# Performance work log

Measured on AMD Instinct MI355X. Metric: run time of the kernel, lower is better.

The kernel has to match this reference:

```python
import jax, jax.numpy as jnp
import numpy as np


def setup_inputs() -> dict:
    key = jax.random.key(0)
    k1, k2 = jax.random.split(key)
    n, g, dim, cb_size = 32768, 4, 128, 512
    x = jax.random.normal(k1, (n, g, dim), dtype=jnp.float32)
    code_book = jax.random.normal(k2, (g, cb_size, dim), dtype=jnp.float32)
    return {"x": x, "code_book": code_book}


def reference(x, code_book):
    # x: (n, g, dim); code_book: (g, cb_size, dim)
    x2 = jnp.sum(x * x, axis=-1, keepdims=True)          # (n, g, 1)
    cb2 = jnp.sum(code_book * code_book, axis=-1)        # (g, cb_size)
    cross = jnp.einsum('gkd,ngd->ngk', code_book, x)     # (n, g, cb_size)
    dist = x2 + cb2 - 2.0 * cross                        # (n, g, cb_size)
    index = jnp.argmin(dist, axis=-1, keepdims=True)     # (n, g, 1) int
    one_hot = jax.nn.one_hot(index[..., 0], code_book.shape[1], dtype=dist.dtype)  # (n, g, cb_size)
    x_hat = jnp.einsum('ngk,gkd->ngd', one_hot, code_book)  # (n, g, dim)
    return (x_hat, one_hot, index)
```

## Files before the change

### kernel.cpp

```cpp
#include <hip/hip_runtime.h>
#include <hip/hip_bf16.h>

#define N_TOT 32768
#define G 4
#define DIM 128
#define CB 512
#define BM 32

#define XHAT_OFF   0
#define ONEHOT_OFF ((size_t)N_TOT * G * DIM)
#define IDX_OFF    (ONEHOT_OFF + (size_t)N_TOT * G * CB)

#define CB2_BYTES    ((size_t)G * CB * 4)
#define CBH_OFF      CB2_BYTES
#define CBHALF_BYTES ((size_t)G * CB * DIM * 2)
#define CBL_OFF      (CBH_OFF + CBHALF_BYTES)
#define WS_NEED      (CBL_OFF + CBHALF_BYTES)

typedef _Float16 half8    __attribute__((ext_vector_type(8)));
typedef _Float16 half4    __attribute__((ext_vector_type(4)));
typedef float    floatx16 __attribute__((ext_vector_type(16)));
typedef float    floatx4  __attribute__((ext_vector_type(4)));

__device__ __forceinline__ void split8(floatx4 v0, floatx4 v1, half8& hi, half8& lo) {
    float f[8] = {v0.x, v0.y, v0.z, v0.w, v1.x, v1.y, v1.z, v1.w};
#pragma unroll
    for (int e = 0; e < 8; ++e) {
        _Float16 h = (_Float16)f[e];
        hi[e] = h;
        lo[e] = (_Float16)(f[e] - (float)h);
    }
}

__global__ void cvq_cb2_kernel(const float* __restrict__ cb, float* __restrict__ cb2h) {
    int i = blockIdx.x * 256 + threadIdx.x;
    if (i >= G * CB) return;
    const float4* p = (const float4*)&cb[(size_t)i * DIM];
    float s = 0.f;
#pragma unroll
    for (int j = 0; j < DIM / 4; ++j) {
        float4 v = p[j];
        s += v.x * v.x + v.y * v.y + v.z * v.z + v.w * v.w;
    }
    cb2h[i] = 0.5f * s;
}

__global__ void cvq_cbpack_kernel(const float* __restrict__ cb,
                                  _Float16* __restrict__ cbfh, _Float16* __restrict__ cbfl) {
    int t = blockIdx.x * 256 + threadIdx.x;
    int col    = t & 31;
    int h      = (t >> 5) & 1;
    int ks     = (t >> 6) & 7;
    int colblk = (t >> 9) & 15;
    int g      = t >> 13;
    const float* src = &cb[((size_t)(g * CB + colblk * 32 + col)) * DIM + ks * 16 + h * 8];
    half8 hi, lo;
    split8(*(const floatx4*)src, *(const floatx4*)(src + 4), hi, lo);
    *(half8*)&cbfh[(size_t)t * 8] = hi;
    *(half8*)&cbfl[(size_t)t * 8] = lo;
}

__global__ __launch_bounds__(256, 3) void cvq_main_packed_kernel(
        const float* __restrict__ x,
        const _Float16* __restrict__ cbfh, const _Float16* __restrict__ cbfl,
        const float* __restrict__ cb, const float* __restrict__ cb2h,
        float* __restrict__ out) {

    __shared__ float xs[BM * DIM];
    __shared__ float part_v[4][BM];
    __shared__ int   part_i[4][BM];
    __shared__ int   idxs[BM];

    const int n0   = blockIdx.x * BM;
    const int g    = blockIdx.y;
    const int tid  = threadIdx.x;
    const int wid  = tid >> 6;
    const int lane = tid & 63;
    const int col  = lane & 31;
    const int h    = lane >> 5;

#pragma unroll
    for (int p = 0; p < 4; ++p) {
        int t = tid + p * 256;
        int r = t >> 5;
        int c = t & 31;
        floatx4 v = *(const floatx4*)&x[(((size_t)(n0 + r)) * G + g) * DIM + (c << 2)];
        *(floatx4*)&xs[r * DIM + ((c ^ (r & 7)) << 2)] = v;
    }
    __syncthreads();

    const size_t cb_base = ((size_t)g * 16 + wid * 4) * 4096 + (size_t)lane * 8;

    floatx16 acc[4] = {};

#pragma unroll
    for (int ks = 0; ks < 8; ++ks) {
        const int c0 = ks * 4 + h * 2;
        const int base = col * DIM;
        const int s = col & 7;
        floatx4 xa = *(const floatx4*)&xs[base + ((c0 ^ s) << 2)];
        floatx4 xb = *(const floatx4*)&xs[base + (((c0 + 1) ^ s) << 2)];
        half8 ah, al;
        split8(xa, xb, ah, al);
#pragma unroll
        for (int t = 0; t < 4; ++t) {
            const size_t o = cb_base + (size_t)t * 4096 + ks * 512;
            half8 bh = *(const half8*)&cbfh[o];
            half8 bl = *(const half8*)&cbfl[o];
            acc[t] = __builtin_amdgcn_mfma_f32_32x32x16_f16(ah, bh, acc[t], 0, 0, 0);
            acc[t] = __builtin_amdgcn_mfma_f32_32x32x16_f16(ah, bl, acc[t], 0, 0, 0);
            acc[t] = __builtin_amdgcn_mfma_f32_32x32x16_f16(al, bh, acc[t], 0, 0, 0);
        }
    }

    float c2v[4];
#pragma unroll
    for (int t = 0; t < 4; ++t)
        c2v[t] = cb2h[g * CB + wid * 128 + t * 32 + col];

#pragma unroll
    for (int r = 0; r < 16; ++r) {
        const int row = (r & 3) + 8 * (r >> 2) + 4 * h;
        float bv = c2v[0] - acc[0][r];
        int   bi = wid * 128 + col;
#pragma unroll
        for (int t = 1; t < 4; ++t) {
            float sc = c2v[t] - acc[t][r];
            int   kk = wid * 128 + t * 32 + col;
            if (sc < bv) { bv = sc; bi = kk; }
        }
#pragma unroll
        for (int off = 1; off < 32; off <<= 1) {
            float ov = __shfl_xor(bv, off);
            int   oi = __shfl_xor(bi, off);
            if (ov < bv || (ov == bv && oi < bi)) { bv = ov; bi = oi; }
        }
        if (col == 0) { part_v[wid][row] = bv; part_i[wid][row] = bi; }
    }
    __syncthreads();

    if (tid < BM) {
        float bv = part_v[0][tid];
        int   bi = part_i[0][tid];
#pragma unroll
        for (int w = 1; w < 4; ++w) {
            float pv = part_v[w][tid];
            int   pi = part_i[w][tid];
            if (pv < bv || (pv == bv && pi < bi)) { bv = pv; bi = pi; }
        }
        idxs[tid] = bi;
        out[IDX_OFF + (size_t)(n0 + tid) * G + g] = (float)bi;
    }
    __syncthreads();

    float* out_xhat = out + XHAT_OFF;
    float* out_oh   = out + ONEHOT_OFF;

#pragma unroll
    for (int p = 0; p < 4; ++p) {
        int t  = tid + p * 256;
        int r  = t >> 5;
        int d4 = (t & 31) << 2;
        int k  = idxs[r];
        floatx4 v = *(const floatx4*)&cb[((size_t)g * CB + k) * DIM + d4];
        __builtin_nontemporal_store(v, (floatx4*)&out_xhat[(((size_t)(n0 + r)) * G + g) * DIM + d4]);
    }

#pragma unroll
    for (int p = 0; p < 16; ++p) {
        int t  = tid + p * 256;
        int r  = t >> 7;
        int k4 = (t & 127) << 2;
        int k  = idxs[r];
        floatx4 v;
        v.x = (k4 + 0 == k) ? 1.f : 0.f;
        v.y = (k4 + 1 == k) ? 1.f : 0.f;
        v.z = (k4 + 2 == k) ? 1.f : 0.f;
        v.w = (k4 + 3 == k) ? 1.f : 0.f;
        __builtin_nontemporal_store(v, (floatx4*)&out_oh[(((size_t)(n0 + r)) * G + g) * CB + k4]);
    }
}

#define FBM 64
__global__ __launch_bounds__(256, 2) void cvq_main_kernel(
        const float* __restrict__ x,
        const float* __restrict__ cb,
        const float* __restrict__ cb2h,
        float* __restrict__ out) {

    __shared__ float part_v[4][FBM];
    __shared__ int   part_i[4][FBM];
    __shared__ int   idxs[FBM];

    const int n0   = blockIdx.x * FBM;
    const int g    = blockIdx.y;
    const int tid  = threadIdx.x;
    const int wid  = tid >> 6;
    const int lane = tid & 63;
    const int col  = lane & 31;
    const int h    = lane >> 5;
    const int klo  = h * 8;

    const float* xr0 = &x[(((size_t)(n0 + col)) * G + g) * DIM + klo];
    const float* xr1 = &x[(((size_t)(n0 + 32 + col)) * G + g) * DIM + klo];
    const float* cbr[4];
#pragma unroll
    for (int t = 0; t < 4; ++t)
        cbr[t] = &cb[((size_t)g * CB + wid * 128 + t * 32 + col) * DIM + klo];

    floatx16 acc[2][4] = {};

#pragma unroll
    for (int ks = 0; ks < 8; ++ks) {
        const int d = ks * 16;
        half8 ah[2], al[2];
        split8(*(const floatx4*)(xr0 + d), *(const floatx4*)(xr0 + d + 4), ah[0], al[0]);
        split8(*(const floatx4*)(xr1 + d), *(const floatx4*)(xr1 + d + 4), ah[1], al[1]);
#pragma unroll
        for (int t = 0; t < 4; ++t) {
            half8 bh, bl;
            split8(*(const floatx4*)(cbr[t] + d), *(const floatx4*)(cbr[t] + d + 4), bh, bl);
#pragma unroll
            for (int mt = 0; mt < 2; ++mt) {
                acc[mt][t] = __builtin_amdgcn_mfma_f32_32x32x16_f16(ah[mt], bh, acc[mt][t], 0, 0, 0);
                acc[mt][t] = __builtin_amdgcn_mfma_f32_32x32x16_f16(ah[mt], bl, acc[mt][t], 0, 0, 0);
                acc[mt][t] = __builtin_amdgcn_mfma_f32_32x32x16_f16(al[mt], bh, acc[mt][t], 0, 0, 0);
            }
        }
    }

    float c2v[4];
#pragma unroll
    for (int t = 0; t < 4; ++t)
        c2v[t] = cb2h[g * CB + wid * 128 + t * 32 + col];

#pragma unroll
    for (int mt = 0; mt < 2; ++mt) {
#pragma unroll
        for (int r = 0; r < 16; ++r) {
            const int row = mt * 32 + (r & 3) + 8 * (r >> 2) + 4 * h;
            float bv = c2v[0] - acc[mt][0][r];
            int   bi = wid * 128 + col;
#pragma unroll
            for (int t = 1; t < 4; ++t) {
                float sc = c2v[t] - acc[mt][t][r];
                int   kk = wid * 128 + t * 32 + col;
                if (sc < bv) { bv = sc; bi = kk; }
            }
#pragma unroll
            for (int off = 1; off < 32; off <<= 1) {
                float ov = __shfl_xor(bv, off);
                int   oi = __shfl_xor(bi, off);
                if (ov < bv || (ov == bv && oi < bi)) { bv = ov; bi = oi; }
            }
            if (col == 0) { part_v[wid][row] = bv; part_i[wid][row] = bi; }
        }
    }
    __syncthreads();

    if (tid < FBM) {
        float bv = part_v[0][tid];
        int   bi = part_i[0][tid];
#pragma unroll
        for (int w = 1; w < 4; ++w) {
            float pv = part_v[w][tid];
            int   pi = part_i[w][tid];
            if (pv < bv || (pv == bv && pi < bi)) { bv = pv; bi = pi; }
        }
        idxs[tid] = bi;
        out[IDX_OFF + (size_t)(n0 + tid) * G + g] = (float)bi;
    }
    __syncthreads();

    float* out_xhat = out + XHAT_OFF;
    float* out_oh   = out + ONEHOT_OFF;

#pragma unroll
    for (int p = 0; p < 8; ++p) {
        int t  = tid + p * 256;
        int r  = t >> 5;
        int d4 = (t & 31) << 2;
        int k  = idxs[r];
        floatx4 v = *(const floatx4*)&cb[((size_t)g * CB + k) * DIM + d4];
        __builtin_nontemporal_store(v, (floatx4*)&out_xhat[(((size_t)(n0 + r)) * G + g) * DIM + d4]);
    }

#pragma unroll
    for (int p = 0; p < 32; ++p) {
        int t  = tid + p * 256;
        int r  = t >> 7;
        int k4 = (t & 127) << 2;
        int k  = idxs[r];
        floatx4 v;
        v.x = (k4 + 0 == k) ? 1.f : 0.f;
        v.y = (k4 + 1 == k) ? 1.f : 0.f;
        v.z = (k4 + 2 == k) ? 1.f : 0.f;
        v.w = (k4 + 3 == k) ? 1.f : 0.f;
        __builtin_nontemporal_store(v, (floatx4*)&out_oh[(((size_t)(n0 + r)) * G + g) * CB + k4]);
    }
}

extern "C" void kernel_launch(void* const* d_in, const int* in_sizes, int n_in,
                              void* d_out, int out_size, void* d_ws, size_t ws_size,
                              hipStream_t stream) {
    const float* x  = (const float*)d_in[0];
    const float* cb = (const float*)d_in[1];
    float* out = (float*)d_out;
    char*  ws  = (char*)d_ws;
    float* cb2h = (float*)ws;

    if (ws_size >= WS_NEED) {
        _Float16* cbfh = (_Float16*)(ws + CBH_OFF);
        _Float16* cbfl = (_Float16*)(ws + CBL_OFF);
        cvq_cb2_kernel<<<dim3((G * CB + 255) / 256), dim3(256), 0, stream>>>(cb, cb2h);
        cvq_cbpack_kernel<<<dim3(G * CB * 16 / 256), dim3(256), 0, stream>>>(cb, cbfh, cbfl);
        cvq_main_packed_kernel<<<dim3(N_TOT / BM, G), dim3(256), 0, stream>>>(x, cbfh, cbfl, cb, cb2h, out);
    } else {
        cvq_cb2_kernel<<<dim3((G * CB + 255) / 256), dim3(256), 0, stream>>>(cb, cb2h);
        cvq_main_kernel<<<dim3(N_TOT / FBM, G), dim3(256), 0, stream>>>(x, cb, cb2h, out);
    }
}
```

Before: 154.6 us.

## Convert VQ main kernel to persistent blocks with register-resident codebook and x prefetch

Replaces the one-tile-per-block kernel with a persistent kernel of 64×4 blocks of 512 threads, each looping over 16 row tiles. Codebook fp16 hi/lo fragments are loaded once into registers and reused across all tiles. The next x tile is prefetched into a double-buffered LDS slot during compute. This removes repeated codebook reloads and block launch overhead, at the cost of high register pressure and fewer resident waves to hide store latency.

After: 210.4 us. +36.1%, slower.

```diff
diff --git a/kernel.cpp b/kernel.cpp
--- a/kernel.cpp
+++ b/kernel.cpp
@@ -6,6 +6,8 @@
 #define DIM 128
 #define CB 512
 #define BM 32
+#define NBX 64
+#define IT (N_TOT / BM / NBX)
 
 #define XHAT_OFF   0
 #define ONEHOT_OFF ((size_t)N_TOT * G * DIM)
@@ -18,7 +20,6 @@
 #define WS_NEED      (CBL_OFF + CBHALF_BYTES)
 
 typedef _Float16 half8    __attribute__((ext_vector_type(8)));
-typedef _Float16 half4    __attribute__((ext_vector_type(4)));
 typedef float    floatx16 __attribute__((ext_vector_type(16)));
 typedef float    floatx4  __attribute__((ext_vector_type(4)));
 
@@ -60,124 +61,146 @@
     *(half8*)&cbfl[(size_t)t * 8] = lo;
 }
 
-__global__ __launch_bounds__(256, 3) void cvq_main_packed_kernel(
+__global__ __launch_bounds__(512, 2) void cvq_persist_kernel(
         const float* __restrict__ x,
         const _Float16* __restrict__ cbfh, const _Float16* __restrict__ cbfl,
         const float* __restrict__ cb, const float* __restrict__ cb2h,
         float* __restrict__ out) {
 
-    __shared__ float xs[BM * DIM];
-    __shared__ float part_v[4][BM];
-    __shared__ int   part_i[4][BM];
+    __shared__ float xs[2][BM * DIM];
+    __shared__ float part_v[8][BM];
+    __shared__ int   part_i[8][BM];
     __shared__ int   idxs[BM];
 
-    const int n0   = blockIdx.x * BM;
     const int g    = blockIdx.y;
+    const int bx   = blockIdx.x;
     const int tid  = threadIdx.x;
     const int wid  = tid >> 6;
     const int lane = tid & 63;
     const int col  = lane & 31;
     const int h    = lane >> 5;
 
-#pragma unroll
-    for (int p = 0; p < 4; ++p) {
-        int t = tid + p * 256;
-        int r = t >> 5;
-        int c = t & 31;
-        floatx4 v = *(const floatx4*)&x[(((size_t)(n0 + r)) * G + g) * DIM + (c << 2)];
-        *(floatx4*)&xs[r * DIM + ((c ^ (r & 7)) << 2)] = v;
-    }
-    __syncthreads();
-
-    const size_t cb_base = ((size_t)g * 16 + wid * 4) * 4096 + (size_t)lane * 8;
-
-    floatx16 acc[4] = {};
-
-#pragma unroll
-    for (int ks = 0; ks < 8; ++ks) {
-        const int c0 = ks * 4 + h * 2;
-        const int base = col * DIM;
-        const int s = col & 7;
-        floatx4 xa = *(const floatx4*)&xs[base + ((c0 ^ s) << 2)];
-        floatx4 xb = *(const floatx4*)&xs[base + (((c0 + 1) ^ s) << 2)];
-        half8 ah, al;
-        split8(xa, xb, ah, al);
-#pragma unroll
-        for (int t = 0; t < 4; ++t) {
-            const size_t o = cb_base + (size_t)t * 4096 + ks * 512;
-            half8 bh = *(const half8*)&cbfh[o];
-            half8 bl = *(const half8*)&cbfl[o];
-            acc[t] = __builtin_amdgcn_mfma_f32_32x32x16_f16(ah, bh, acc[t], 0, 0, 0);
-            acc[t] = __builtin_amdgcn_mfma_f32_32x32x16_f16(ah, bl, acc[t], 0, 0, 0);
-            acc[t] = __builtin_amdgcn_mfma_f32_32x32x16_f16(al, bh, acc[t], 0, 0, 0);
-        }
-    }
-
-    float c2v[4];
-#pragma unroll
-    for (int t = 0; t < 4; ++t)
-        c2v[t] = cb2h[g * CB + wid * 128 + t * 32 + col];
-
-#pragma unroll
-    for (int r = 0; r < 16; ++r) {
-        const int row = (r & 3) + 8 * (r >> 2) + 4 * h;
-        float bv = c2v[0] - acc[0][r];
-        int   bi = wid * 128 + col;
-#pragma unroll
-        for (int t = 1; t < 4; ++t) {
-            float sc = c2v[t] - acc[t][r];
-            int   kk = wid * 128 + t * 32 + col;
-            if (sc < bv) { bv = sc; bi = kk; }
-        }
-#pragma unroll
-        for (int off = 1; off < 32; off <<= 1) {
-            float ov = __shfl_xor(bv, off);
-            int   oi = __shfl_xor(bi, off);
-            if (ov < bv || (ov == bv && oi < bi)) { bv = ov; bi = oi; }
-        }
-        if (col == 0) { part_v[wid][row] = bv; part_i[wid][row] = bi; }
-    }
-    __syncthreads();
-
-    if (tid < BM) {
-        float bv = part_v[0][tid];
-        int   bi = part_i[0][tid];
-#pragma unroll
-        for (int w = 1; w < 4; ++w) {
-            float pv = part_v[w][tid];
-            int   pi = part_i[w][tid];
-            if (pv < bv || (pv == bv && pi < bi)) { bv = pv; bi = pi; }
-        }
-        idxs[tid] = bi;
-        out[IDX_OFF + (size_t)(n0 + tid) * G + g] = (float)bi;
-    }
-    __syncthreads();
+    half8 bhf[2][8], blf[2][8];
+#pragma unroll
+    for (int t = 0; t < 2; ++t)
+#pragma unroll
+        for (int ks = 0; ks < 8; ++ks) {
+            const size_t o = ((size_t)(g * 16 + wid * 2 + t)) * 4096 + ks * 512 + (size_t)lane * 8;
+            bhf[t][ks] = *(const half8*)&cbfh[o];
+            blf[t][ks] = *(const half8*)&cbfl[o];
+        }
+
+    const float c2v0 = cb2h[g * CB + wid * 64 + col];
+    const float c2v1 = cb2h[g * CB + wid * 64 + 32 + col];
+
+    const int sr  = tid >> 5;
+    const int sc  = tid & 31;
+    const int ssl = sr * DIM + ((sc ^ (sr & 7)) << 2);
 
     float* out_xhat = out + XHAT_OFF;
     float* out_oh   = out + ONEHOT_OFF;
 
-#pragma unroll
-    for (int p = 0; p < 4; ++p) {
-        int t  = tid + p * 256;
-        int r  = t >> 5;
-        int d4 = (t & 31) << 2;
-        int k  = idxs[r];
-        floatx4 v = *(const floatx4*)&cb[((size_t)g * CB + k) * DIM + d4];
-        __builtin_nontemporal_store(v, (floatx4*)&out_xhat[(((size_t)(n0 + r)) * G + g) * DIM + d4]);
-    }
-
-#pragma unroll
-    for (int p = 0; p < 16; ++p) {
-        int t  = tid + p * 256;
-        int r  = t >> 7;
-        int k4 = (t & 127) << 2;
-        int k  = idxs[r];
-        floatx4 v;
-        v.x = (k4 + 0 == k) ? 1.f : 0.f;
-        v.y = (k4 + 1 == k) ? 1.f : 0.f;
-        v.z = (k4 + 2 == k) ? 1.f : 0.f;
-        v.w = (k4 + 3 == k) ? 1.f : 0.f;
-        __builtin_nontemporal_store(v, (floatx4*)&out_oh[(((size_t)(n0 + r)) * G + g) * CB + k4]);
+    {
+        const float* p = &x[(((size_t)bx * BM + sr) * G + g) * DIM + (sc << 2)];
+        floatx4 s0 = *(const floatx4*)p;
+        floatx4 s1 = *(const floatx4*)(p + (size_t)16 * G * DIM);
+        *(floatx4*)&xs[0][ssl] = s0;
+        *(floatx4*)&xs[0][ssl + 16 * DIM] = s1;
+    }
+    __syncthreads();
+
+    int cur = 0;
+    for (int it = 0; it < IT; ++it) {
+        const size_t n0 = ((size_t)it * NBX + bx) * BM;
+
+        floatx4 s0, s1;
+        if (it + 1 < IT) {
+            const size_t nn = ((size_t)(it + 1) * NBX + bx) * BM;
+            const float* p = &x[((nn + sr) * G + g) * DIM + (sc << 2)];
+            s0 = *(const floatx4*)p;
+            s1 = *(const floatx4*)(p + (size_t)16 * G * DIM);
+        }
+
+        floatx16 acc[2] = {};
+#pragma unroll
+        for (int ks = 0; ks < 8; ++ks) {
+            const int c0 = ks * 4 + h * 2;
+            const int s  = col & 7;
+            const float* xb = &xs[cur][col * DIM];
+            floatx4 xa = *(const floatx4*)&xb[((c0 ^ s) << 2)];
+            floatx4 xc = *(const floatx4*)&xb[(((c0 + 1) ^ s) << 2)];
+            half8 ah, al;
+            split8(xa, xc, ah, al);
+#pragma unroll
+            for (int t = 0; t < 2; ++t) {
+                acc[t] = __builtin_amdgcn_mfma_f32_32x32x16_f16(ah, bhf[t][ks], acc[t], 0, 0, 0);
+                acc[t] = __builtin_amdgcn_mfma_f32_32x32x16_f16(ah, blf[t][ks], acc[t], 0, 0, 0);
+                acc[t] = __builtin_amdgcn_mfma_f32_32x32x16_f16(al, bhf[t][ks], acc[t], 0, 0, 0);
+            }
+        }
+
+#pragma unroll
+        for (int r = 0; r < 16; ++r) {
+            const int row = (r & 3) + 8 * (r >> 2) + 4 * h;
+            float bv = c2v0 - acc[0][r];
+            int   bi = wid * 64 + col;
+            float s1v = c2v1 - acc[1][r];
+            int   k1  = wid * 64 + 32 + col;
+            if (s1v < bv) { bv = s1v; bi = k1; }
+#pragma unroll
+            for (int off = 1; off < 32; off <<= 1) {
+                float ov = __shfl_xor(bv, off);
+                int   oi = __shfl_xor(bi, off);
+                if (ov < bv || (ov == bv && oi < bi)) { bv = ov; bi = oi; }
+            }
+            if (col == 0) { part_v[wid][row] = bv; part_i[wid][row] = bi; }
+        }
+        __syncthreads();
+
+        if (it + 1 < IT) {
+            *(floatx4*)&xs[cur ^ 1][ssl] = s0;
+            *(floatx4*)&xs[cur ^ 1][ssl + 16 * DIM] = s1;
+        }
+
+        if (tid < BM) {
+            float bv = part_v[0][tid];
+            int   bi = part_i[0][tid];
+#pragma unroll
+            for (int w = 1; w < 8; ++w) {
+                float pv = part_v[w][tid];
+                int   pi = part_i[w][tid];
+                if (pv < bv || (pv == bv && pi < bi)) { bv = pv; bi = pi; }
+            }
+            idxs[tid] = bi;
+            out[IDX_OFF + (n0 + tid) * G + g] = (float)bi;
+        }
+        __syncthreads();
+
+#pragma unroll
+        for (int p = 0; p < 2; ++p) {
+            int t  = tid + p * 512;
+            int r  = t >> 5;
+            int d4 = (t & 31) << 2;
+            int k  = idxs[r];
+            floatx4 v = *(const floatx4*)&cb[((size_t)g * CB + k) * DIM + d4];
+            __builtin_nontemporal_store(v, (floatx4*)&out_xhat[((n0 + r) * G + g) * DIM + d4]);
+        }
+
+#pragma unroll
+        for (int p = 0; p < 8; ++p) {
+            int t  = tid + p * 512;
+            int r  = t >> 7;
+            int k4 = (t & 127) << 2;
+            int k  = idxs[r];
+            floatx4 v;
+            v.x = (k4 + 0 == k) ? 1.f : 0.f;
+            v.y = (k4 + 1 == k) ? 1.f : 0.f;
+            v.z = (k4 + 2 == k) ? 1.f : 0.f;
+            v.w = (k4 + 3 == k) ? 1.f : 0.f;
+            __builtin_nontemporal_store(v, (floatx4*)&out_oh[((n0 + r) * G + g) * CB + k4]);
+        }
+
+        cur ^= 1;
     }
 }
 
@@ -314,7 +337,7 @@
         _Float16* cbfl = (_Float16*)(ws + CBL_OFF);
         cvq_cb2_kernel<<<dim3((G * CB + 255) / 256), dim3(256), 0, stream>>>(cb, cb2h);
         cvq_cbpack_kernel<<<dim3(G * CB * 16 / 256), dim3(256), 0, stream>>>(cb, cbfh, cbfl);
-        cvq_main_packed_kernel<<<dim3(N_TOT / BM, G), dim3(256), 0, stream>>>(x, cbfh, cbfl, cb, cb2h, out);
+        cvq_persist_kernel<<<dim3(NBX, G), dim3(512), 0, stream>>>(x, cbfh, cbfl, cb, cb2h, out);
     } else {
         cvq_cb2_kernel<<<dim3((G * CB + 255) / 256), dim3(256), 0, stream>>>(cb, cb2h);
         cvq_main_kernel<<<dim3(N_TOT / FBM, G), dim3(256), 0, stream>>>(x, cb, cb2h, out);
```

## Double-buffer codebook fragments in LDS via async global-to-LDS loads

Applied to the files above, without the earlier changes.

The main kernel now stages the packed fp16 hi/lo codebook fragments through a double-buffered LDS area using direct global-to-LDS loads. Each k-slice is prefetched while MFMAs run on the previous one, replacing the direct global fragment loads. The x tile is split into hi/lo fp16 once, held in registers for all k-steps, and its staging buffer is reused for the codebook. This costs a block barrier per k-step, more LDS (64 KB plus partials), and more registers, and occupancy is lowered from 3 to 2 blocks.

Measured after the change: 181.7 us. +17.5%, slower.

```diff
diff --git a/kernel.cpp b/kernel.cpp
--- a/kernel.cpp
+++ b/kernel.cpp
@@ -18,9 +18,14 @@
 #define WS_NEED      (CBL_OFF + CBHALF_BYTES)
 
 typedef _Float16 half8    __attribute__((ext_vector_type(8)));
-typedef _Float16 half4    __attribute__((ext_vector_type(4)));
 typedef float    floatx16 __attribute__((ext_vector_type(16)));
 typedef float    floatx4  __attribute__((ext_vector_type(4)));
+
+__device__ __forceinline__ void gload_lds16(void* lds, const void* g) {
+    __builtin_amdgcn_global_load_lds(
+        (const __attribute__((address_space(1))) unsigned int*)g,
+        (__attribute__((address_space(3))) unsigned int*)lds, 16, 0, 0);
+}
 
 __device__ __forceinline__ void split8(floatx4 v0, floatx4 v1, half8& hi, half8& lo) {
     float f[8] = {v0.x, v0.y, v0.z, v0.w, v1.x, v1.y, v1.z, v1.w};
@@ -60,13 +65,13 @@
     *(half8*)&cbfl[(size_t)t * 8] = lo;
 }
 
-__global__ __launch_bounds__(256, 3) void cvq_main_packed_kernel(
+__global__ __launch_bounds__(256, 2) void cvq_pipe_kernel(
         const float* __restrict__ x,
         const _Float16* __restrict__ cbfh, const _Float16* __restrict__ cbfl,
         const float* __restrict__ cb, const float* __restrict__ cb2h,
         float* __restrict__ out) {
 
-    __shared__ float xs[BM * DIM];
+    __shared__ _Float16 cbuf[2][16384];
     __shared__ float part_v[4][BM];
     __shared__ int   part_i[4][BM];
     __shared__ int   idxs[BM];
@@ -79,38 +84,63 @@
     const int col  = lane & 31;
     const int h    = lane >> 5;
 
+    float* xstage = (float*)cbuf[0];
 #pragma unroll
     for (int p = 0; p < 4; ++p) {
         int t = tid + p * 256;
         int r = t >> 5;
         int c = t & 31;
         floatx4 v = *(const floatx4*)&x[(((size_t)(n0 + r)) * G + g) * DIM + (c << 2)];
-        *(floatx4*)&xs[r * DIM + ((c ^ (r & 7)) << 2)] = v;
-    }
-    __syncthreads();
-
-    const size_t cb_base = ((size_t)g * 16 + wid * 4) * 4096 + (size_t)lane * 8;
+        *(floatx4*)&xstage[r * DIM + ((c ^ (r & 7)) << 2)] = v;
+    }
+    __syncthreads();
+
+    half8 ah[8], al[8];
+    {
+        const float* xb = &xstage[col * DIM];
+        const int s = col & 7;
+#pragma unroll
+        for (int ks = 0; ks < 8; ++ks) {
+            const int c0 = ks * 4 + h * 2;
+            floatx4 xa = *(const floatx4*)&xb[((c0 ^ s) << 2)];
+            floatx4 xc = *(const floatx4*)&xb[(((c0 + 1) ^ s) << 2)];
+            split8(xa, xc, ah[ks], al[ks]);
+        }
+    }
+    __syncthreads();
+
+    const _Float16* pb[2] = { cbfh + ((size_t)g * 16 + wid * 4) * 4096 + lane * 8,
+                              cbfl + ((size_t)g * 16 + wid * 4) * 4096 + lane * 8 };
+
+#define ISSUE_KS(ksv, buf)                                                      \
+    {                                                                           \
+        _Float16* dst = &cbuf[buf][(size_t)wid * 4096];                         \
+        _Pragma("unroll")                                                       \
+        for (int j = 0; j < 8; ++j) {                                           \
+            const _Float16* gp = pb[j & 1] + (size_t)(j >> 1) * 4096 + (ksv) * 512; \
+            gload_lds16((void*)(dst + j * 512), (const void*)gp);               \
+        }                                                                       \
+    }
+
+    ISSUE_KS(0, 0);
+    __syncthreads();
 
     floatx16 acc[4] = {};
 
-#pragma unroll
     for (int ks = 0; ks < 8; ++ks) {
-        const int c0 = ks * 4 + h * 2;
-        const int base = col * DIM;
-        const int s = col & 7;
-        floatx4 xa = *(const floatx4*)&xs[base + ((c0 ^ s) << 2)];
-        floatx4 xb = *(const floatx4*)&xs[base + (((c0 + 1) ^ s) << 2)];
-        half8 ah, al;
-        split8(xa, xb, ah, al);
+        const int cur = ks & 1;
+        if (ks < 7) ISSUE_KS(ks + 1, cur ^ 1);
+
+        const _Float16* rb = &cbuf[cur][(size_t)wid * 4096 + lane * 8];
 #pragma unroll
         for (int t = 0; t < 4; ++t) {
-            const size_t o = cb_base + (size_t)t * 4096 + ks * 512;
-            half8 bh = *(const half8*)&cbfh[o];
-            half8 bl = *(const half8*)&cbfl[o];
-            acc[t] = __builtin_amdgcn_mfma_f32_32x32x16_f16(ah, bh, acc[t], 0, 0, 0);
-            acc[t] = __builtin_amdgcn_mfma_f32_32x32x16_f16(ah, bl, acc[t], 0, 0, 0);
-            acc[t] = __builtin_amdgcn_mfma_f32_32x32x16_f16(al, bh, acc[t], 0, 0, 0);
-        }
+            half8 bh = *(const half8*)(rb + (size_t)t * 1024);
+            half8 bl = *(const half8*)(rb + (size_t)t * 1024 + 512);
+            acc[t] = __builtin_amdgcn_mfma_f32_32x32x16_f16(ah[ks], bh, acc[t], 0, 0, 0);
+            acc[t] = __builtin_amdgcn_mfma_f32_32x32x16_f16(ah[ks], bl, acc[t], 0, 0, 0);
+            acc[t] = __builtin_amdgcn_mfma_f32_32x32x16_f16(al[ks], bh, acc[t], 0, 0, 0);
+        }
+        __syncthreads();
     }
 
     float c2v[4];
@@ -314,7 +344,7 @@
         _Float16* cbfl = (_Float16*)(ws + CBL_OFF);
         cvq_cb2_kernel<<<dim3((G * CB + 255) / 256), dim3(256), 0, stream>>>(cb, cb2h);
         cvq_cbpack_kernel<<<dim3(G * CB * 16 / 256), dim3(256), 0, stream>>>(cb, cbfh, cbfl);
-        cvq_main_packed_kernel<<<dim3(N_TOT / BM, G), dim3(256), 0, stream>>>(x, cbfh, cbfl, cb, cb2h, out);
+        cvq_pipe_kernel<<<dim3(N_TOT / BM, G), dim3(256), 0, stream>>>(x, cbfh, cbfl, cb, cb2h, out);
     } else {
         cvq_cb2_kernel<<<dim3((G * CB + 255) / 256), dim3(256), 0, stream>>>(cb, cb2h);
         cvq_main_kernel<<<dim3(N_TOT / FBM, G), dim3(256), 0, stream>>>(x, cb, cb2h, out);
```

## Double rows per block and offload one-hot zeroing to memset

Applied to the files above, without the earlier changes.

Raises the packed kernel's row tile from 32 to 64 so each wave reuses every loaded codebook fragment across two MFMA row tiles, halving codebook traffic per row. Drops the per-block one-hot write loop: a hipMemsetAsync zeroes the whole one-hot buffer beforehand, and the kernel scatters a single 1.0 per row. This trades the kernel's vectorized zero stores for a separate memset pass. It also raises register pressure, with occupancy bounds lowered from 3 to 2.

New measurement: 192.0 us. 1.24x slower.

```diff
diff --git a/kernel.cpp b/kernel.cpp
--- a/kernel.cpp
+++ b/kernel.cpp
@@ -5,11 +5,12 @@
 #define G 4
 #define DIM 128
 #define CB 512
-#define BM 32
+#define BM 64
 
 #define XHAT_OFF   0
 #define ONEHOT_OFF ((size_t)N_TOT * G * DIM)
 #define IDX_OFF    (ONEHOT_OFF + (size_t)N_TOT * G * CB)
+#define ONEHOT_BYTES ((size_t)N_TOT * G * CB * 4)
 
 #define CB2_BYTES    ((size_t)G * CB * 4)
 #define CBH_OFF      CB2_BYTES
@@ -18,7 +19,6 @@
 #define WS_NEED      (CBL_OFF + CBHALF_BYTES)
 
 typedef _Float16 half8    __attribute__((ext_vector_type(8)));
-typedef _Float16 half4    __attribute__((ext_vector_type(4)));
 typedef float    floatx16 __attribute__((ext_vector_type(16)));
 typedef float    floatx4  __attribute__((ext_vector_type(4)));
 
@@ -60,13 +60,13 @@
     *(half8*)&cbfl[(size_t)t * 8] = lo;
 }
 
-__global__ __launch_bounds__(256, 3) void cvq_main_packed_kernel(
+__global__ __launch_bounds__(256, 2) void cvq_main64_kernel(
         const float* __restrict__ x,
         const _Float16* __restrict__ cbfh, const _Float16* __restrict__ cbfl,
         const float* __restrict__ cb, const float* __restrict__ cb2h,
         float* __restrict__ out) {
 
-    __shared__ float xs[BM * DIM];
+    __shared__ float xstage[BM * DIM];
     __shared__ float part_v[4][BM];
     __shared__ int   part_i[4][BM];
     __shared__ int   idxs[BM];
@@ -80,36 +80,41 @@
     const int h    = lane >> 5;
 
 #pragma unroll
-    for (int p = 0; p < 4; ++p) {
+    for (int p = 0; p < 8; ++p) {
         int t = tid + p * 256;
         int r = t >> 5;
         int c = t & 31;
         floatx4 v = *(const floatx4*)&x[(((size_t)(n0 + r)) * G + g) * DIM + (c << 2)];
-        *(floatx4*)&xs[r * DIM + ((c ^ (r & 7)) << 2)] = v;
+        *(floatx4*)&xstage[r * DIM + ((c ^ (r & 7)) << 2)] = v;
     }
     __syncthreads();
 
     const size_t cb_base = ((size_t)g * 16 + wid * 4) * 4096 + (size_t)lane * 8;
 
-    floatx16 acc[4] = {};
+    floatx16 acc[2][4] = {};
 
 #pragma unroll
     for (int ks = 0; ks < 8; ++ks) {
         const int c0 = ks * 4 + h * 2;
-        const int base = col * DIM;
-        const int s = col & 7;
-        floatx4 xa = *(const floatx4*)&xs[base + ((c0 ^ s) << 2)];
-        floatx4 xb = *(const floatx4*)&xs[base + (((c0 + 1) ^ s) << 2)];
-        half8 ah, al;
-        split8(xa, xb, ah, al);
+        const int s  = col & 7;
+        const float* xb0 = &xstage[col * DIM];
+        const float* xb1 = &xstage[(col + 32) * DIM];
+        half8 ah[2], al[2];
+        split8(*(const floatx4*)&xb0[((c0 ^ s) << 2)],
+               *(const floatx4*)&xb0[(((c0 + 1) ^ s) << 2)], ah[0], al[0]);
+        split8(*(const floatx4*)&xb1[((c0 ^ s) << 2)],
+               *(const floatx4*)&xb1[(((c0 + 1) ^ s) << 2)], ah[1], al[1]);
 #pragma unroll
         for (int t = 0; t < 4; ++t) {
             const size_t o = cb_base + (size_t)t * 4096 + ks * 512;
             half8 bh = *(const half8*)&cbfh[o];
             half8 bl = *(const half8*)&cbfl[o];
-            acc[t] = __builtin_amdgcn_mfma_f32_32x32x16_f16(ah, bh, acc[t], 0, 0, 0);
-            acc[t] = __builtin_amdgcn_mfma_f32_32x32x16_f16(ah, bl, acc[t], 0, 0, 0);
-            acc[t] = __builtin_amdgcn_mfma_f32_32x32x16_f16(al, bh, acc[t], 0, 0, 0);
+#pragma unroll
+            for (int mt = 0; mt < 2; ++mt) {
+                acc[mt][t] = __builtin_amdgcn_mfma_f32_32x32x16_f16(ah[mt], bh, acc[mt][t], 0, 0, 0);
+                acc[mt][t] = __builtin_amdgcn_mfma_f32_32x32x16_f16(ah[mt], bl, acc[mt][t], 0, 0, 0);
+                acc[mt][t] = __builtin_amdgcn_mfma_f32_32x32x16_f16(al[mt], bh, acc[mt][t], 0, 0, 0);
+            }
         }
     }
 
@@ -119,23 +124,26 @@
         c2v[t] = cb2h[g * CB + wid * 128 + t * 32 + col];
 
 #pragma unroll
-    for (int r = 0; r < 16; ++r) {
-        const int row = (r & 3) + 8 * (r >> 2) + 4 * h;
-        float bv = c2v[0] - acc[0][r];
-        int   bi = wid * 128 + col;
-#pragma unroll
-        for (int t = 1; t < 4; ++t) {
-            float sc = c2v[t] - acc[t][r];
-            int   kk = wid * 128 + t * 32 + col;
-            if (sc < bv) { bv = sc; bi = kk; }
-        }
-#pragma unroll
-        for (int off = 1; off < 32; off <<= 1) {
-            float ov = __shfl_xor(bv, off);
-            int   oi = __shfl_xor(bi, off);
-            if (ov < bv || (ov == bv && oi < bi)) { bv = ov; bi = oi; }
-        }
-        if (col == 0) { part_v[wid][row] = bv; part_i[wid][row] = bi; }
+    for (int mt = 0; mt < 2; ++mt) {
+#pragma unroll
+        for (int r = 0; r < 16; ++r) {
+            const int row = mt * 32 + (r & 3) + 8 * (r >> 2) + 4 * h;
+            float bv = c2v[0] - acc[mt][0][r];
+            int   bi = wid * 128 + col;
+#pragma unroll
+            for (int t = 1; t < 4; ++t) {
+                float sc = c2v[t] - acc[mt][t][r];
+                int   kk = wid * 128 + t * 32 + col;
+                if (sc < bv) { bv = sc; bi = kk; }
+            }
+#pragma unroll
+            for (int off = 1; off < 32; off <<= 1) {
+                float ov = __shfl_xor(bv, off);
+                int   oi = __shfl_xor(bi, off);
+                if (ov < bv || (ov == bv && oi < bi)) { bv = ov; bi = oi; }
+            }
+            if (col == 0) { part_v[wid][row] = bv; part_i[wid][row] = bi; }
+        }
     }
     __syncthreads();
 
@@ -150,34 +158,19 @@
         }
         idxs[tid] = bi;
         out[IDX_OFF + (size_t)(n0 + tid) * G + g] = (float)bi;
+        out[ONEHOT_OFF + ((size_t)(n0 + tid) * G + g) * CB + bi] = 1.0f;
     }
     __syncthreads();
 
     float* out_xhat = out + XHAT_OFF;
-    float* out_oh   = out + ONEHOT_OFF;
-
-#pragma unroll
-    for (int p = 0; p < 4; ++p) {
+#pragma unroll
+    for (int p = 0; p < 8; ++p) {
         int t  = tid + p * 256;
         int r  = t >> 5;
         int d4 = (t & 31) << 2;
         int k  = idxs[r];
         floatx4 v = *(const floatx4*)&cb[((size_t)g * CB + k) * DIM + d4];
         __builtin_nontemporal_store(v, (floatx4*)&out_xhat[(((size_t)(n0 + r)) * G + g) * DIM + d4]);
-    }
-
-#pragma unroll
-    for (int p = 0; p < 16; ++p) {
-        int t  = tid + p * 256;
-        int r  = t >> 7;
-        int k4 = (t & 127) << 2;
-        int k  = idxs[r];
-        floatx4 v;
-        v.x = (k4 + 0 == k) ? 1.f : 0.f;
-        v.y = (k4 + 1 == k) ? 1.f : 0.f;
-        v.z = (k4 + 2 == k) ? 1.f : 0.f;
-        v.w = (k4 + 3 == k) ? 1.f : 0.f;
-        __builtin_nontemporal_store(v, (floatx4*)&out_oh[(((size_t)(n0 + r)) * G + g) * CB + k4]);
     }
 }
 
@@ -314,7 +307,8 @@
         _Float16* cbfl = (_Float16*)(ws + CBL_OFF);
         cvq_cb2_kernel<<<dim3((G * CB + 255) / 256), dim3(256), 0, stream>>>(cb, cb2h);
         cvq_cbpack_kernel<<<dim3(G * CB * 16 / 256), dim3(256), 0, stream>>>(cb, cbfh, cbfl);
-        cvq_main_packed_kernel<<<dim3(N_TOT / BM, G), dim3(256), 0, stream>>>(x, cbfh, cbfl, cb, cb2h, out);
+        hipMemsetAsync(out + ONEHOT_OFF, 0, ONEHOT_BYTES, stream);
+        cvq_main64_kernel<<<dim3(N_TOT / BM, G), dim3(256), 0, stream>>>(x, cbfh, cbfl, cb, cb2h, out);
     } else {
         cvq_cb2_kernel<<<dim3((G * CB + 255) / 256), dim3(256), 0, stream>>>(cb, cb2h);
         cvq_main_kernel<<<dim3(N_TOT / FBM, G), dim3(256), 0, stream>>>(x, cb, cb2h, out);
```
